# Performance work log

Measured on AMD Instinct MI355X. Metric: run time of the kernel, lower is better.

The kernel has to match this reference:

```python
import jax, jax.numpy as jnp
import numpy as np

V, E = 50000, 800000
D_NODE, D_EDGE, D_OUT = 64, 32, 64
SLOPE = 0.2


def setup_inputs() -> dict:
    key = jax.random.key(0)
    ks = jax.random.split(key, 12)
    inp = {
        "node_feats": jax.random.normal(ks[0], (V, D_NODE), dtype=jnp.float32),
        "edge_feats": jax.random.normal(ks[1], (E, D_EDGE), dtype=jnp.float32),
        "edge_index": jax.random.randint(ks[2], (2, E), 0, V, dtype=jnp.int64),
        "W_q": jax.random.normal(ks[3], (D_NODE, D_OUT), dtype=jnp.float32) / np.sqrt(D_NODE),
        "b_q": jax.random.normal(ks[4], (D_OUT,), dtype=jnp.float32) * 0.02,
        "W_k": jax.random.normal(ks[5], (D_NODE, D_OUT), dtype=jnp.float32) / np.sqrt(D_NODE),
        "b_k": jax.random.normal(ks[6], (D_OUT,), dtype=jnp.float32) * 0.02,
        "W_v": jax.random.normal(ks[7], (D_NODE, D_OUT), dtype=jnp.float32) / np.sqrt(D_NODE),
        "b_v": jax.random.normal(ks[8], (D_OUT,), dtype=jnp.float32) * 0.02,
        "W_e": jax.random.normal(ks[9], (D_EDGE, D_OUT), dtype=jnp.float32) / np.sqrt(D_EDGE),
        "b_e": jax.random.normal(ks[10], (D_OUT,), dtype=jnp.float32) * 0.02,
        "a_w": jax.random.normal(ks[11], (D_OUT, 1), dtype=jnp.float32) / np.sqrt(D_OUT),
        "a_b": jnp.zeros((1,), dtype=jnp.float32),
    }
    return inp


def reference(node_feats, edge_feats, edge_index, W_q, b_q, W_k, b_k, W_v, b_v, W_e, b_e, a_w, a_b):
    src, dest = edge_index[0], edge_index[1]
    n_nodes = node_feats.shape[0]

    # per-edge projections: [E, d_o]
    Q = node_feats[src] @ W_q + b_q
    K = node_feats[dest] @ W_k + b_k
    Vv = node_feats[dest] @ W_v + b_v
    bias = edge_feats @ W_e + b_e

    pre = Q + K + bias
    act = jnp.where(pre >= 0, pre, SLOPE * pre)  # LeakyReLU
    scores = act @ a_w + a_b  # [E, 1]

    # scatter-softmax over destination node (dim 0)
    seg_max = jax.ops.segment_max(scores, dest, num_segments=n_nodes)  # [V,1]
    ex = jnp.exp(scores - seg_max[dest])
    denom = jax.ops.segment_sum(ex, dest, num_segments=n_nodes)  # [V,1]
    alpha = ex / denom[dest]  # [E,1]

    # scatter-sum aggregation
    node_hiddens = jax.ops.segment_sum(alpha * Vv, dest, num_segments=n_nodes)
    return node_hiddens
```

## Files before the change

### kernel.cpp

```cpp
#include <hip/hip_runtime.h>


#define D 64

__global__ void zero_flags_kernel(unsigned int* __restrict__ f, int nwords) {
    int i = blockIdx.x * blockDim.x + threadIdx.x;
    if (i < nwords) f[i] = 0u;
}

__global__ void mark_dest_kernel(const int* __restrict__ dest,
                                 unsigned char* __restrict__ flag,
                                 int E, int V) {
    int i = blockIdx.x * blockDim.x + threadIdx.x;
    if (i < E) {
        int d = dest[i];
        if ((unsigned)d < (unsigned)V) flag[d] = 1;
    }
}

__global__ __launch_bounds__(256) void proj_v_kernel(
        const float* __restrict__ nf,
        const float* __restrict__ Wv,
        const float* __restrict__ bv,
        const unsigned char* __restrict__ flag,
        float* __restrict__ out,
        int V) {
    const int lane = threadIdx.x & 63;
    const int wave = threadIdx.x >> 6;

    float w[D];
#pragma unroll
    for (int l = 0; l < D; ++l) w[l] = Wv[l * D + lane];
    const float b = bv[lane];

    const int waveId = blockIdx.x * 4 + wave;
    const int nWaves = gridDim.x * 4;

    for (int v = waveId; v < V; v += nWaves) {
        const float x = nf[(size_t)v * D + lane];
        float acc = b;
#pragma unroll
        for (int l = 0; l < D; ++l)
            acc = fmaf(__shfl(x, l, 64), w[l], acc);
        out[(size_t)v * D + lane] = flag[v] ? acc : 0.0f;
    }
}

extern "C" void kernel_launch(void* const* d_in, const int* in_sizes, int n_in,
                              void* d_out, int out_size, void* d_ws, size_t ws_size,
                              hipStream_t stream) {
    const float* nf = (const float*)d_in[0];
    const int* eidx = (const int*)d_in[2];
    const float* Wv = (const float*)d_in[7];
    const float* bv = (const float*)d_in[8];
    float* out = (float*)d_out;

    const int V = in_sizes[0] / D;
    const int E = in_sizes[2] / 2;

    unsigned char* flags = (unsigned char*)d_ws;
    const int nwords = (V + 3) / 4;

    zero_flags_kernel<<<(nwords + 255) / 256, 256, 0, stream>>>(
        (unsigned int*)d_ws, nwords);
    mark_dest_kernel<<<(E + 255) / 256, 256, 0, stream>>>(
        eidx + E, flags, E, V);
    proj_v_kernel<<<2048, 256, 0, stream>>>(nf, Wv, bv, flags, out, V);
}
```

Before: 199.1 us.

## Switch V projection from wave-per-node shuffles to thread-per-node register GEMV

Reworks the projection kernel so each thread owns one node. It loads that node's 64 features into registers with float4 loads and reads the weights as wave-uniform values, which removes the 64 cross-lane shuffles per node. Outputs are written in 16-column chunks as float4 stores, and the grid is now sized to one thread per node instead of a fixed grid-stride loop. The trade-off is that row-strided per-thread global loads and stores are less coalesced. The grid also shrinks to only about 196 blocks, which may underfill the GPU.

```diff
diff --git a/kernel.cpp b/kernel.cpp
--- a/kernel.cpp
+++ b/kernel.cpp
@@ -27,22 +27,43 @@
         int V) {
     const int lane = threadIdx.x & 63;
     const int wave = threadIdx.x >> 6;
+    const int v    = (blockIdx.x * 4 + wave) * 64 + lane;
+    const bool valid = (v < V);
+    const int vc = valid ? v : (V - 1);
 
-    float w[D];
+    float x[D];
+    const float4* xr = reinterpret_cast<const float4*>(nf + (size_t)vc * D);
 #pragma unroll
-    for (int l = 0; l < D; ++l) w[l] = Wv[l * D + lane];
-    const float b = bv[lane];
+    for (int m = 0; m < 16; ++m) {
+        float4 t = xr[m];
+        x[4 * m + 0] = t.x; x[4 * m + 1] = t.y;
+        x[4 * m + 2] = t.z; x[4 * m + 3] = t.w;
+    }
 
-    const int waveId = blockIdx.x * 4 + wave;
-    const int nWaves = gridDim.x * 4;
+    const float keep = (valid && flag[vc]) ? 1.0f : 0.0f;
 
-    for (int v = waveId; v < V; v += nWaves) {
-        const float x = nf[(size_t)v * D + lane];
-        float acc = b;
+    float* orow = out + (size_t)vc * D;
+
 #pragma unroll
-        for (int l = 0; l < D; ++l)
-            acc = fmaf(__shfl(x, l, 64), w[l], acc);
-        out[(size_t)v * D + lane] = flag[v] ? acc : 0.0f;
+    for (int cc = 0; cc < 4; ++cc) {
+        float acc[16];
+#pragma unroll
+        for (int c = 0; c < 16; ++c) acc[c] = bv[cc * 16 + c];
+#pragma unroll
+        for (int k = 0; k < D; ++k) {
+            const float xk = x[k];
+            const float* wrow = Wv + k * D + cc * 16;
+#pragma unroll
+            for (int c = 0; c < 16; ++c)
+                acc[c] = fmaf(xk, wrow[c], acc[c]);
+        }
+        if (valid) {
+            float4* o4 = reinterpret_cast<float4*>(orow + cc * 16);
+#pragma unroll
+            for (int q = 0; q < 4; ++q)
+                o4[q] = make_float4(acc[4 * q + 0] * keep, acc[4 * q + 1] * keep,
+                                    acc[4 * q + 2] * keep, acc[4 * q + 3] * keep);
+        }
     }
 }
 
@@ -65,5 +86,6 @@
         (unsigned int*)d_ws, nwords);
     mark_dest_kernel<<<(E + 255) / 256, 256, 0, stream>>>(
         eidx + E, flags, E, V);
-    proj_v_kernel<<<2048, 256, 0, stream>>>(nf, Wv, bv, flags, out, V);
+    proj_v_kernel<<<(V + 255) / 256, 256, 0, stream>>>(
+        nf, Wv, bv, flags, out, V);
 }
```

Result: no change. 197.8 us (-0.7%).

## Compute V projection with split-bf16 MFMA instead of shuffle FMAs

Applied to the files above, without the earlier changes.

Replaces the per-lane shuffle/FMA matvec with 16x16x32 bf16 MFMA instructions, using a hi/lo bf16 split (three products) to approximate fp32 accuracy. Each wave now handles one 16-row tile and converts the weight matrix into bf16 fragments itself. This targets the ALU/shuffle cost of the projection, at the cost of redundant per-wave weight loading and conversion and slightly reduced precision.

```diff
diff --git a/kernel.cpp b/kernel.cpp
--- a/kernel.cpp
+++ b/kernel.cpp
@@ -2,6 +2,19 @@
 
 
 #define D 64
+
+typedef short bf16x8 __attribute__((ext_vector_type(8)));
+typedef float f32x4  __attribute__((ext_vector_type(4)));
+
+__device__ __forceinline__ unsigned short f32_to_bf16_rne(float f) {
+    union { float f; unsigned int u; } c; c.f = f;
+    unsigned int r = c.u + 0x7FFFu + ((c.u >> 16) & 1u);
+    return (unsigned short)(r >> 16);
+}
+__device__ __forceinline__ float bf16_bits_to_f32(unsigned short b) {
+    union { unsigned int u; float f; } c; c.u = ((unsigned int)b) << 16;
+    return c.f;
+}
 
 __global__ void zero_flags_kernel(unsigned int* __restrict__ f, int nwords) {
     int i = blockIdx.x * blockDim.x + threadIdx.x;
@@ -18,7 +31,7 @@
     }
 }
 
-__global__ __launch_bounds__(256) void proj_v_kernel(
+__global__ __launch_bounds__(256) void proj_v_mfma_kernel(
         const float* __restrict__ nf,
         const float* __restrict__ Wv,
         const float* __restrict__ bv,
@@ -27,22 +40,68 @@
         int V) {
     const int lane = threadIdx.x & 63;
     const int wave = threadIdx.x >> 6;
+    const int n16  = lane & 15;
+    const int quad = lane >> 4;
 
-    float w[D];
+    const int v0 = (blockIdx.x * 4 + wave) * 16;
+    if (v0 >= V) return;
+
+    bf16x8 Bhi[2][4], Blo[2][4];
 #pragma unroll
-    for (int l = 0; l < D; ++l) w[l] = Wv[l * D + lane];
-    const float b = bv[lane];
+    for (int kt = 0; kt < 2; ++kt)
+#pragma unroll
+        for (int nt = 0; nt < 4; ++nt)
+#pragma unroll
+            for (int j = 0; j < 8; ++j) {
+                float w = Wv[(kt * 32 + quad * 8 + j) * D + nt * 16 + n16];
+                unsigned short hi = f32_to_bf16_rne(w);
+                float rem = w - bf16_bits_to_f32(hi);
+                Bhi[kt][nt][j] = (short)hi;
+                Blo[kt][nt][j] = (short)f32_to_bf16_rne(rem);
+            }
 
-    const int waveId = blockIdx.x * 4 + wave;
-    const int nWaves = gridDim.x * 4;
+    const float* xrow = nf + (size_t)(v0 + n16) * D;
+    bf16x8 Ahi[2], Alo[2];
+#pragma unroll
+    for (int kt = 0; kt < 2; ++kt) {
+        const float4* p = reinterpret_cast<const float4*>(xrow + kt * 32 + quad * 8);
+        float4 a = p[0], b = p[1];
+        float xs[8] = {a.x, a.y, a.z, a.w, b.x, b.y, b.z, b.w};
+#pragma unroll
+        for (int j = 0; j < 8; ++j) {
+            unsigned short hi = f32_to_bf16_rne(xs[j]);
+            float rem = xs[j] - bf16_bits_to_f32(hi);
+            Ahi[kt][j] = (short)hi;
+            Alo[kt][j] = (short)f32_to_bf16_rne(rem);
+        }
+    }
 
-    for (int v = waveId; v < V; v += nWaves) {
-        const float x = nf[(size_t)v * D + lane];
-        float acc = b;
+    f32x4 acc[4];
 #pragma unroll
-        for (int l = 0; l < D; ++l)
-            acc = fmaf(__shfl(x, l, 64), w[l], acc);
-        out[(size_t)v * D + lane] = flag[v] ? acc : 0.0f;
+    for (int nt = 0; nt < 4; ++nt) {
+        float b = bv[nt * 16 + n16];
+        acc[nt] = (f32x4){b, b, b, b};
+    }
+
+#pragma unroll
+    for (int kt = 0; kt < 2; ++kt)
+#pragma unroll
+        for (int nt = 0; nt < 4; ++nt) {
+            acc[nt] = __builtin_amdgcn_mfma_f32_16x16x32_bf16(
+                Ahi[kt], Bhi[kt][nt], acc[nt], 0, 0, 0);
+            acc[nt] = __builtin_amdgcn_mfma_f32_16x16x32_bf16(
+                Ahi[kt], Blo[kt][nt], acc[nt], 0, 0, 0);
+            acc[nt] = __builtin_amdgcn_mfma_f32_16x16x32_bf16(
+                Alo[kt], Bhi[kt][nt], acc[nt], 0, 0, 0);
+        }
+
+#pragma unroll
+    for (int r = 0; r < 4; ++r) {
+        const int v = v0 + quad * 4 + r;
+        const float keep = flag[v] ? 1.0f : 0.0f;
+#pragma unroll
+        for (int nt = 0; nt < 4; ++nt)
+            out[(size_t)v * D + nt * 16 + n16] = acc[nt][r] * keep;
     }
 }
 
@@ -65,5 +124,6 @@
         (unsigned int*)d_ws, nwords);
     mark_dest_kernel<<<(E + 255) / 256, 256, 0, stream>>>(
         eidx + E, flags, E, V);
-    proj_v_kernel<<<2048, 256, 0, stream>>>(nf, Wv, bv, flags, out, V);
+    proj_v_mfma_kernel<<<(V + 63) / 64, 256, 0, stream>>>(
+        nf, Wv, bv, flags, out, V);
 }
```

Result: faster. 173.8 us (-12.7%).
